# Kernel optimization log

Measured on AMD Instinct MI355X. Metric: run time of the kernel, lower is better.

The kernel has to match this reference:

```python
import jax, jax.numpy as jnp
import numpy as np

N, E, F_IN, F_OUT = 8192, 1024, 256, 256


def setup_inputs() -> dict:
    key = jax.random.key(0)
    k1, k2, k3, k4 = jax.random.split(key, 4)
    X = jax.random.normal(k1, (N, F_IN), dtype=jnp.float32)
    # binary incidence matrix: node i belongs to hyperedge j with p=0.05
    H = (jax.random.uniform(k2, (N, E)) < 0.05).astype(jnp.float32)
    W = jax.random.normal(k3, (F_OUT, F_IN), dtype=jnp.float32) * (1.0 / np.sqrt(F_IN))
    b = jax.random.normal(k4, (F_OUT,), dtype=jnp.float32) * 0.01
    return {"X": X, "H": H, "W": W, "b": b}


def reference(X, H, W, b):
    # Dv = diag(row sums of H), De = diag(col sums of H)
    dv = jnp.sum(H, axis=1)                      # [N] node degrees
    de = jnp.sum(H, axis=0)                      # [E] edge degrees
    dv_inv_sqrt = 1.0 / jnp.sqrt(dv)             # inv of sqrt(Dv) (diagonal)
    de_inv = 1.0 / de                            # inv of De (diagonal)
    # diagonal matrices realized as broadcast scalings (same math, no N x N).
    Xs = X * dv_inv_sqrt[:, None]
    M = H.T @ Xs                                 # H^T (...)          [E, F]
    M = M * de_inv[:, None]                      # De^-1 (...)        [E, F]
    X_new = (H @ M) * dv_inv_sqrt[:, None]       # Dv^-1/2 H (...)    [N, F]
    return X_new @ W.T + b                       # nn.Linear
```

## Files before the change

kernel.cpp:

```cpp
#include <hip/hip_runtime.h>
#include <hip/hip_bf16.h>
#include <stdint.h>

typedef __attribute__((ext_vector_type(8))) short bf16x8;
typedef __attribute__((ext_vector_type(4))) float f32x4;
typedef __attribute__((ext_vector_type(4))) unsigned int u32x4;
typedef __attribute__((ext_vector_type(2))) unsigned int u32x2;
typedef unsigned short u16;
typedef unsigned int u32;
typedef unsigned char u8;
typedef unsigned long long u64;

#define N_NODES 8192
#define N_EDGES 1024
#define F_DIM   256

__device__ __forceinline__ u16 f2bf(float f) {
    union { float f; u32 u; } v; v.f = f;
    u32 u = v.u;
    u = (u + 0x7FFFu + ((u >> 16) & 1u)) >> 16;
    return (u16)u;
}

__device__ __forceinline__ void async16(const u16* g, u16* l) {
    __builtin_amdgcn_global_load_lds(
        (const __attribute__((address_space(1))) u32*)(const void*)g,
        (__attribute__((address_space(3))) u32*)(void*)l, 16, 0, 0);
}

__device__ __forceinline__ bf16x8 expand8(u32 byte) {
    union { u32 u[4]; bf16x8 v; } r;
#pragma unroll
    for (int i = 0; i < 4; ++i)
        r.u[i] = (((byte >> (2 * i)) & 1u) ? 0x3F80u : 0u)
               | (((byte >> (2 * i + 1)) & 1u) ? 0x3F800000u : 0u);
    return r.v;
}

__global__ __launch_bounds__(512) void prep(
    const float* __restrict__ H, const float* __restrict__ X,
    const float* __restrict__ W,
    float* __restrict__ dv, u16* __restrict__ Xsb,
    u32* __restrict__ HbTs, u32* __restrict__ HbN, u16* __restrict__ Wb) {
    __shared__ u16 hmask[32][68];
    const int tid = threadIdx.x;
    const int wv = tid >> 6;
    const int lane = tid & 63;
    const int blk = blockIdx.x;
    const int n0 = blk * 32 + wv * 4;

    f32x4 hv[4][4], xv[4];
#pragma unroll
    for (int r = 0; r < 4; ++r) {
        const int n = n0 + r;
#pragma unroll
        for (int q = 0; q < 4; ++q)
            hv[r][q] = *(const f32x4*)(&H[(size_t)n * N_EDGES + q * 256 + lane * 4]);
        xv[r] = *(const f32x4*)(&X[(size_t)n * F_DIM + lane * 4]);
    }

    if (wv == 7) {
        const f32x4 w = *(const f32x4*)(&W[(size_t)blk * F_DIM + lane * 4]);
        u32x2 pk;
        pk[0] = (u32)f2bf(w[0]) | ((u32)f2bf(w[1]) << 16);
        pk[1] = (u32)f2bf(w[2]) | ((u32)f2bf(w[3]) << 16);
        *(u32x2*)(&Wb[(size_t)blk * F_DIM + lane * 4]) = pk;
    }

#pragma unroll
    for (int r = 0; r < 4; ++r) {
        const int n = n0 + r;
        u32 m16 = 0u;
#pragma unroll
        for (int q = 0; q < 4; ++q)
#pragma unroll
            for (int j = 0; j < 4; ++j)
                m16 |= ((hv[r][q][j] != 0.f) ? 1u : 0u) << (q * 4 + j);
        hmask[wv * 4 + r][lane] = (u16)m16;
        u32 s = (u32)__popc(m16);
#pragma unroll
        for (int d = 1; d < 64; d <<= 1) s += __shfl_xor(s, d, 64);
        if (lane == 0) dv[n] = (float)s;
        const float sc = rsqrtf((float)s);
        u32x2 pk;
        pk[0] = (u32)f2bf(xv[r][0] * sc) | ((u32)f2bf(xv[r][1] * sc) << 16);
        pk[1] = (u32)f2bf(xv[r][2] * sc) | ((u32)f2bf(xv[r][3] * sc) << 16);
        *(u32x2*)(&Xsb[(size_t)n * F_DIM + lane * 4]) = pk;
    }
    __syncthreads();
    {
        u32x2 st;
#pragma unroll
        for (int eo = 0; eo < 2; ++eo) {
            const int e = tid * 2 + eo;
            const int widx = (e & 255) >> 2;
            const int bit = ((e >> 8) << 2) + (e & 3);
            u32 w = 0u;
#pragma unroll
            for (int r = 0; r < 32; ++r)
                w |= (u32)((hmask[r][widx] >> bit) & 1u) << r;
            st[eo] = w;
        }
        *(u32x2*)(&HbTs[(size_t)blk * N_EDGES + tid * 2]) = st;
    }
    {
        const int r = tid & 31;
        const int wec = tid >> 5;
#pragma unroll
        for (int wo = 0; wo < 2; ++wo) {
            const int we = wec + wo * 16;
            const int q = we >> 3, l0 = (we & 7) * 8;
            const u32x2 a = *(const u32x2*)(&hmask[r][l0]);
            const u32x2 b2 = *(const u32x2*)(&hmask[r][l0 + 4]);
            const u32 sh = q * 4;
            u32 w = ((a[0] >> sh) & 0xFu)
                  | (((a[0] >> (16 + sh)) & 0xFu) << 4)
                  | (((a[1] >> sh) & 0xFu) << 8)
                  | (((a[1] >> (16 + sh)) & 0xFu) << 12)
                  | (((b2[0] >> sh) & 0xFu) << 16)
                  | (((b2[0] >> (16 + sh)) & 0xFu) << 20)
                  | (((b2[1] >> sh) & 0xFu) << 24)
                  | (((b2[1] >> (16 + sh)) & 0xFu) << 28);
            HbN[(size_t)we * N_NODES + blk * 32 + r] = w;
        }
    }
}

__global__ __launch_bounds__(256) void gemmZ(
    const u16* __restrict__ Wb, const u16* __restrict__ Xsb,
    u16* __restrict__ Zt) {
    __shared__ __align__(16) u16 As[64 * 64];
    __shared__ __align__(16) u16 Bs[64 * 64];
    const int tid = threadIdx.x;
    const int lane = tid & 63;
    const int wave = tid >> 6;
    const int wm = wave >> 1, wn = wave & 1;
    const int row16 = lane & 15;
    const int quad = lane >> 4;
    const int row0 = blockIdx.y * 64;
    const int col0 = blockIdx.x * 64;
    const int srow = lane >> 3;
    const int scol = (lane & 7) * 8;
    const u16* gA0 = Wb + (size_t)(row0 + wave * 16 + srow) * F_DIM + scol;
    const u16* gB0 = Xsb + (size_t)(col0 + wave * 16 + srow) * F_DIM + scol;
    const size_t rstep8 = (size_t)8 * F_DIM;
    u16* lA0 = &As[(wave * 16) * 64];
    u16* lB0 = &Bs[(wave * 16) * 64];

    f32x4 acc[2][2] = {};
    for (int k = 0; k < 256; k += 64) {
        async16(gA0 + k, lA0);
        async16(gA0 + k + rstep8, lA0 + 8 * 64);
        async16(gB0 + k, lB0);
        async16(gB0 + k + rstep8, lB0 + 8 * 64);
        __syncthreads();
#pragma unroll
        for (int ks = 0; ks < 2; ++ks) {
            bf16x8 af[2], bfr[2];
#pragma unroll
            for (int t = 0; t < 2; ++t) {
                af[t]  = *(const bf16x8*)(&As[(wm * 32 + t * 16 + row16) * 64 + ks * 32 + quad * 8]);
                bfr[t] = *(const bf16x8*)(&Bs[(wn * 32 + t * 16 + row16) * 64 + ks * 32 + quad * 8]);
            }
#pragma unroll
            for (int tm = 0; tm < 2; tm++)
#pragma unroll
                for (int tn = 0; tn < 2; tn++)
                    acc[tm][tn] = __builtin_amdgcn_mfma_f32_16x16x32_bf16(
                        af[tm], bfr[tn], acc[tm][tn], 0, 0, 0);
        }
        __syncthreads();
    }
#pragma unroll
    for (int tm = 0; tm < 2; tm++)
#pragma unroll
        for (int tn = 0; tn < 2; tn++) {
            const int col = col0 + wn * 32 + tn * 16 + row16;
#pragma unroll
            for (int r = 0; r < 4; r++) {
                const int row = row0 + wm * 32 + tm * 16 + quad * 4 + r;
                Zt[(size_t)row * N_NODES + col] = f2bf(acc[tm][tn][r]);
            }
        }
}

__global__ __launch_bounds__(512) void gemmM2(
    const u16* __restrict__ Zt, const u32* __restrict__ HbTs,
    u16* __restrict__ M2t) {
    __shared__ __align__(16) u8 smem[65536];
    __shared__ float cnts[8][2][16];
    const int tid = threadIdx.x;
    const int wv = tid >> 6, lane = tid & 63;
    const int f0 = ((int)blockIdx.x & 7) * 32;
    const int e0 = ((int)blockIdx.x >> 3) * 32;
    const int row16 = lane & 15, quad = lane >> 4;
    const int srow = lane & 15, schunk = lane >> 4;
    u16* myBs = (u16*)(smem + wv * 8192);
    const int kbase = wv * 1024;

    f32x4 acc[2][2] = {};
    u32 cnt0 = 0, cnt1 = 0;
    u32 wA[2][2], wB[2][2];

    auto STAGE = [&](int it, int buf) {
        __builtin_amdgcn_sched_barrier(0);
        const int k0 = kbase + it * 64;
#pragma unroll
        for (int tn = 0; tn < 2; ++tn)
#pragma unroll
            for (int ks = 0; ks < 2; ++ks)
                async16(Zt + (size_t)(f0 + tn * 16 + srow) * N_NODES + k0 + ks * 32 + schunk * 8,
                        myBs + buf * 2048 + (tn * 2 + ks) * 512);
    };
    auto LOADW = [&](int it, u32 (&w)[2][2]) {
        const int k0 = kbase + it * 64;
#pragma unroll
        for (int tm = 0; tm < 2; ++tm)
#pragma unroll
            for (int ks = 0; ks < 2; ++ks)
                w[tm][ks] = HbTs[(size_t)((k0 >> 5) + ks) * N_EDGES + e0 + tm * 16 + row16];
    };
    auto COMPUTE = [&](int buf, u32 (&w)[2][2]) {
        asm volatile("s_waitcnt vmcnt(4)" ::: "memory");
        __builtin_amdgcn_sched_barrier(0);
#pragma unroll
        for (int ks = 0; ks < 2; ++ks) {
            bf16x8 bfr[2];
#pragma unroll
            for (int tn = 0; tn < 2; ++tn)
                bfr[tn] = *(const bf16x8*)(myBs + buf * 2048 + (tn * 2 + ks) * 512 + lane * 8);
#pragma unroll
            for (int tm = 0; tm < 2; ++tm) {
                const u32 byte = (w[tm][ks] >> (quad * 8)) & 0xFFu;
                if (tm == 0) cnt0 += (u32)__popc(byte); else cnt1 += (u32)__popc(byte);
                const bf16x8 af = expand8(byte);
#pragma unroll
                for (int tn = 0; tn < 2; ++tn)
                    acc[tm][tn] = __builtin_amdgcn_mfma_f32_16x16x32_bf16(
                        af, bfr[tn], acc[tm][tn], 0, 0, 0);
            }
        }
    };

    STAGE(0, 0);
    LOADW(0, wA);
    for (int i = 0; i < 8; ++i) {
        STAGE(2 * i + 1, 1);
        LOADW(2 * i + 1, wB);
        COMPUTE(0, wA);
        const int nxt = (2 * i + 2 < 16) ? (2 * i + 2) : 15;
        STAGE(nxt, 0);
        LOADW(nxt, wA);
        COMPUTE(1, wB);
    }

    cnt0 += __shfl_down(cnt0, 32, 64); cnt0 += __shfl_down(cnt0, 16, 64);
    cnt1 += __shfl_down(cnt1, 32, 64); cnt1 += __shfl_down(cnt1, 16, 64);
    if (lane < 16) {
        cnts[wv][0][lane] = (float)cnt0;
        cnts[wv][1][lane] = (float)cnt1;
    }
    __syncthreads();
    {
        float* redf = (float*)smem;
        float* my = &redf[(size_t)(wv * 64 + lane) * 17];
#pragma unroll
        for (int tm = 0; tm < 2; ++tm)
#pragma unroll
            for (int tn = 0; tn < 2; ++tn)
#pragma unroll
                for (int r = 0; r < 4; ++r)
                    my[tm * 8 + tn * 4 + r] = acc[tm][tn][r];
    }
    __syncthreads();
    {
        const float* redf = (const float*)smem;
#pragma unroll
        for (int h = 0; h < 2; ++h) {
            const int idx = tid + h * 512;
            const int fl = idx >> 5, el = idx & 31;
            const int tm = el >> 4, q = (el >> 2) & 3, r = el & 3;
            const int tn = fl >> 4, r16 = fl & 15;
            const int srcl = q * 16 + r16;
            const int j = tm * 8 + tn * 4 + r;
            float s = 0.f, de = 0.f;
#pragma unroll
            for (int w = 0; w < 8; ++w) {
                s += redf[(size_t)(w * 64 + srcl) * 17 + j];
                de += cnts[w][tm][el & 15];
            }
            M2t[(size_t)(f0 + fl) * N_EDGES + e0 + el] = f2bf(s / de);
        }
    }
}

__global__ __launch_bounds__(512) void gemmOUT(
    const u16* __restrict__ M2t, const u32* __restrict__ HbN,
    const float* __restrict__ dv, const float* __restrict__ bias,
    float* __restrict__ out) {
    __shared__ __align__(16) u16 Bs[32 * 1028];
    const int tid = threadIdx.x;
    const int wv = tid >> 6, lane = tid & 63;
    const int row16 = lane & 15, quad = lane >> 4;
    const int j0 = ((int)blockIdx.x & 7) * 32;
    const int ng = ((int)blockIdx.x >> 3) * 256 + wv * 32;

#pragma unroll
    for (int rr = 0; rr < 4; ++rr) {
        const int jr = wv * 4 + rr;
#pragma unroll
        for (int c = 0; c < 2; ++c)
            async16(M2t + (size_t)(j0 + jr) * N_EDGES + c * 512 + lane * 8,
                    &Bs[jr * 1028 + c * 512]);
    }
    __syncthreads();

    f32x4 acc[2][2] = {};
    u32 wA[2][2], wB[2][2];
    auto LOADW = [&](int it, u32 (&w)[2][2]) {
#pragma unroll
        for (int tm = 0; tm < 2; ++tm)
#pragma unroll
            for (int ks = 0; ks < 2; ++ks)
                w[tm][ks] = HbN[(size_t)(it * 2 + ks) * N_NODES + ng + tm * 16 + row16];
    };
    auto COMPUTE = [&](int it, u32 (&w)[2][2]) {
#pragma unroll
        for (int ks = 0; ks < 2; ++ks) {
            bf16x8 bfr[2];
#pragma unroll
            for (int tn = 0; tn < 2; ++tn) {
                const int base = (tn * 16 + row16) * 1028 + it * 64 + ks * 32 + quad * 8;
                union { u32x2 lo_hi[2]; bf16x8 v; } u;
                u.lo_hi[0] = *(const u32x2*)(&Bs[base]);
                u.lo_hi[1] = *(const u32x2*)(&Bs[base + 4]);
                bfr[tn] = u.v;
            }
#pragma unroll
            for (int tm = 0; tm < 2; ++tm) {
                const u32 byte = (w[tm][ks] >> (quad * 8)) & 0xFFu;
                const bf16x8 af = expand8(byte);
#pragma unroll
                for (int tn = 0; tn < 2; ++tn)
                    acc[tm][tn] = __builtin_amdgcn_mfma_f32_16x16x32_bf16(
                        af, bfr[tn], acc[tm][tn], 0, 0, 0);
            }
        }
    };

    LOADW(0, wA);
    for (int i = 0; i < 8; ++i) {
        LOADW(2 * i + 1, wB);
        COMPUTE(2 * i, wA);
        const int nxt = (2 * i + 2 < 16) ? (2 * i + 2) : 15;
        LOADW(nxt, wA);
        COMPUTE(2 * i + 1, wB);
    }

#pragma unroll
    for (int tm = 0; tm < 2; ++tm)
#pragma unroll
        for (int tn = 0; tn < 2; ++tn) {
            const int col = j0 + tn * 16 + row16;
            const float bc = bias[col];
#pragma unroll
            for (int r = 0; r < 4; ++r) {
                const int n = ng + tm * 16 + quad * 4 + r;
                out[(size_t)n * F_DIM + col] = acc[tm][tn][r] * rsqrtf(dv[n]) + bc;
            }
        }
}

extern "C" void kernel_launch(void* const* d_in, const int* in_sizes, int n_in,
                              void* d_out, int out_size, void* d_ws, size_t ws_size,
                              hipStream_t stream) {
    (void)in_sizes; (void)n_in; (void)out_size; (void)ws_size;
    const float* X = (const float*)d_in[0];
    const float* H = (const float*)d_in[1];
    const float* W = (const float*)d_in[2];
    const float* b = (const float*)d_in[3];
    float* out = (float*)d_out;

    char* ws = (char*)d_ws;
    float* dv   = (float*)(ws);
    u32*   HbTs = (u32*)(ws + 0x10000);
    u32*   HbN  = (u32*)(ws + 0x110000);
    u16*   Wb   = (u16*)(ws + 0x210000);
    u16*   Xsb  = (u16*)(ws + 0x230000);
    u16*   Zt   = (u16*)(ws + 0x630000);
    u16*   M2t  = (u16*)(ws + 0xA30000);

    prep<<<256, 512, 0, stream>>>(H, X, W, dv, Xsb, HbTs, HbN, Wb);
    gemmZ<<<dim3(128, 4), 256, 0, stream>>>(Wb, Xsb, Zt);
    gemmM2<<<256, 512, 0, stream>>>(Zt, HbTs, M2t);
    gemmOUT<<<256, 512, 0, stream>>>(M2t, HbN, dv, b, out);
}
```

Measured before the change: 121.8 us.

## Fuse the X·Wᵀ GEMM into the prep kernel and drop the gemmZ launch

The separate gemmZ kernel is removed. Each prep block now keeps its 32 scaled bf16 X rows in LDS and computes their product with W directly using MFMA, writing the transposed Zt tile. This removes one kernel launch and the round trip of Xsb and Wb through global memory. In exchange, every block re-reads the full fp32 W matrix from global or cache and converts it to bf16, and prep gains extra LDS use and register pressure.

```diff
diff --git a/kernel.cpp b/kernel.cpp
--- a/kernel.cpp
+++ b/kernel.cpp
@@ -40,9 +40,10 @@
 __global__ __launch_bounds__(512) void prep(
     const float* __restrict__ H, const float* __restrict__ X,
     const float* __restrict__ W,
-    float* __restrict__ dv, u16* __restrict__ Xsb,
-    u32* __restrict__ HbTs, u32* __restrict__ HbN, u16* __restrict__ Wb) {
+    float* __restrict__ dv, u32* __restrict__ HbTs, u32* __restrict__ HbN,
+    u16* __restrict__ Zt) {
     __shared__ u16 hmask[32][68];
+    __shared__ u16 Xls[32][264];
     const int tid = threadIdx.x;
     const int wv = tid >> 6;
     const int lane = tid & 63;
@@ -57,14 +58,6 @@
         for (int q = 0; q < 4; ++q)
             hv[r][q] = *(const f32x4*)(&H[(size_t)n * N_EDGES + q * 256 + lane * 4]);
         xv[r] = *(const f32x4*)(&X[(size_t)n * F_DIM + lane * 4]);
-    }
-
-    if (wv == 7) {
-        const f32x4 w = *(const f32x4*)(&W[(size_t)blk * F_DIM + lane * 4]);
-        u32x2 pk;
-        pk[0] = (u32)f2bf(w[0]) | ((u32)f2bf(w[1]) << 16);
-        pk[1] = (u32)f2bf(w[2]) | ((u32)f2bf(w[3]) << 16);
-        *(u32x2*)(&Wb[(size_t)blk * F_DIM + lane * 4]) = pk;
     }
 
 #pragma unroll
@@ -85,7 +78,7 @@
         u32x2 pk;
         pk[0] = (u32)f2bf(xv[r][0] * sc) | ((u32)f2bf(xv[r][1] * sc) << 16);
         pk[1] = (u32)f2bf(xv[r][2] * sc) | ((u32)f2bf(xv[r][3] * sc) << 16);
-        *(u32x2*)(&Xsb[(size_t)n * F_DIM + lane * 4]) = pk;
+        *(u32x2*)(&Xls[wv * 4 + r][lane * 4]) = pk;
     }
     __syncthreads();
     {
@@ -124,64 +117,42 @@
             HbN[(size_t)we * N_NODES + blk * 32 + r] = w;
         }
     }
-}
-
-__global__ __launch_bounds__(256) void gemmZ(
-    const u16* __restrict__ Wb, const u16* __restrict__ Xsb,
-    u16* __restrict__ Zt) {
-    __shared__ __align__(16) u16 As[64 * 64];
-    __shared__ __align__(16) u16 Bs[64 * 64];
-    const int tid = threadIdx.x;
-    const int lane = tid & 63;
-    const int wave = tid >> 6;
-    const int wm = wave >> 1, wn = wave & 1;
-    const int row16 = lane & 15;
-    const int quad = lane >> 4;
-    const int row0 = blockIdx.y * 64;
-    const int col0 = blockIdx.x * 64;
-    const int srow = lane >> 3;
-    const int scol = (lane & 7) * 8;
-    const u16* gA0 = Wb + (size_t)(row0 + wave * 16 + srow) * F_DIM + scol;
-    const u16* gB0 = Xsb + (size_t)(col0 + wave * 16 + srow) * F_DIM + scol;
-    const size_t rstep8 = (size_t)8 * F_DIM;
-    u16* lA0 = &As[(wave * 16) * 64];
-    u16* lB0 = &Bs[(wave * 16) * 64];
-
-    f32x4 acc[2][2] = {};
-    for (int k = 0; k < 256; k += 64) {
-        async16(gA0 + k, lA0);
-        async16(gA0 + k + rstep8, lA0 + 8 * 64);
-        async16(gB0 + k, lB0);
-        async16(gB0 + k + rstep8, lB0 + 8 * 64);
-        __syncthreads();
-#pragma unroll
-        for (int ks = 0; ks < 2; ++ks) {
-            bf16x8 af[2], bfr[2];
-#pragma unroll
-            for (int t = 0; t < 2; ++t) {
-                af[t]  = *(const bf16x8*)(&As[(wm * 32 + t * 16 + row16) * 64 + ks * 32 + quad * 8]);
-                bfr[t] = *(const bf16x8*)(&Bs[(wn * 32 + t * 16 + row16) * 64 + ks * 32 + quad * 8]);
-            }
-#pragma unroll
-            for (int tm = 0; tm < 2; tm++)
-#pragma unroll
-                for (int tn = 0; tn < 2; tn++)
+    {
+        const int row16 = lane & 15, quad = lane >> 4;
+        f32x4 acc[2][2] = {};
+#pragma unroll
+        for (int ks = 0; ks < 8; ++ks) {
+            bf16x8 af[2];
+#pragma unroll
+            for (int tm = 0; tm < 2; ++tm)
+                af[tm] = *(const bf16x8*)(&Xls[tm * 16 + row16][ks * 32 + quad * 8]);
+#pragma unroll
+            for (int tn = 0; tn < 2; ++tn) {
+                const int j = wv * 32 + tn * 16 + row16;
+                const f32x4 w0 = *(const f32x4*)(&W[(size_t)j * F_DIM + ks * 32 + quad * 8]);
+                const f32x4 w1 = *(const f32x4*)(&W[(size_t)j * F_DIM + ks * 32 + quad * 8 + 4]);
+                union { u32x4 u; bf16x8 v; } bu;
+                bu.u[0] = (u32)f2bf(w0[0]) | ((u32)f2bf(w0[1]) << 16);
+                bu.u[1] = (u32)f2bf(w0[2]) | ((u32)f2bf(w0[3]) << 16);
+                bu.u[2] = (u32)f2bf(w1[0]) | ((u32)f2bf(w1[1]) << 16);
+                bu.u[3] = (u32)f2bf(w1[2]) | ((u32)f2bf(w1[3]) << 16);
+#pragma unroll
+                for (int tm = 0; tm < 2; ++tm)
                     acc[tm][tn] = __builtin_amdgcn_mfma_f32_16x16x32_bf16(
-                        af[tm], bfr[tn], acc[tm][tn], 0, 0, 0);
-        }
-        __syncthreads();
-    }
-#pragma unroll
-    for (int tm = 0; tm < 2; tm++)
-#pragma unroll
-        for (int tn = 0; tn < 2; tn++) {
-            const int col = col0 + wn * 32 + tn * 16 + row16;
-#pragma unroll
-            for (int r = 0; r < 4; r++) {
-                const int row = row0 + wm * 32 + tm * 16 + quad * 4 + r;
-                Zt[(size_t)row * N_NODES + col] = f2bf(acc[tm][tn][r]);
-            }
-        }
+                        af[tm], bu.v, acc[tm][tn], 0, 0, 0);
+            }
+        }
+#pragma unroll
+        for (int tm = 0; tm < 2; ++tm)
+#pragma unroll
+            for (int tn = 0; tn < 2; ++tn) {
+                const int j = wv * 32 + tn * 16 + row16;
+                u32x2 pk;
+                pk[0] = (u32)f2bf(acc[tm][tn][0]) | ((u32)f2bf(acc[tm][tn][1]) << 16);
+                pk[1] = (u32)f2bf(acc[tm][tn][2]) | ((u32)f2bf(acc[tm][tn][3]) << 16);
+                *(u32x2*)(&Zt[(size_t)j * N_NODES + blk * 32 + tm * 16 + quad * 4]) = pk;
+            }
+    }
 }
 
 __global__ __launch_bounds__(512) void gemmM2(
@@ -385,13 +356,10 @@
     float* dv   = (float*)(ws);
     u32*   HbTs = (u32*)(ws + 0x10000);
     u32*   HbN  = (u32*)(ws + 0x110000);
-    u16*   Wb   = (u16*)(ws + 0x210000);
-    u16*   Xsb  = (u16*)(ws + 0x230000);
-    u16*   Zt   = (u16*)(ws + 0x630000);
-    u16*   M2t  = (u16*)(ws + 0xA30000);
-
-    prep<<<256, 512, 0, stream>>>(H, X, W, dv, Xsb, HbTs, HbN, Wb);
-    gemmZ<<<dim3(128, 4), 256, 0, stream>>>(Wb, Xsb, Zt);
+    u16*   Zt   = (u16*)(ws + 0x210000);
+    u16*   M2t  = (u16*)(ws + 0x610000);
+
+    prep<<<256, 512, 0, stream>>>(H, X, W, dv, HbTs, HbN, Zt);
     gemmM2<<<256, 512, 0, stream>>>(Zt, HbTs, M2t);
     gemmOUT<<<256, 512, 0, stream>>>(M2t, HbN, dv, b, out);
 }
```

Result: no change. 122.3 us (+0.4%).
